# Optimization experiments

Measured on AMD Instinct MI355X. Metric: run time of the kernel, lower is better.

## Reference

```python
import jax, jax.numpy as jnp
import numpy as np

N = 1_000_000
DATA_DIM = 16
N_COND = 8            # conditions 1..8; condition 0 uses the base model (id 0)
N_BUCKETS = 8         # uniform time intervals per condition on [0,1)
N_MODELS = N_COND * N_BUCKETS + 1   # 65, matches num_models+1 in the torch ctor
HIDDEN = 6            # SimpleModel(data_dim, hidden=6, time_embed_dim=6)
IN_DIM = DATA_DIM + 1 # MLP input is cat([data, t], dim=1)


def setup_inputs() -> dict:
    key = jax.random.key(0)
    k_data, k_cond, k_t, k_w1, k_b1, k_w2, k_b2 = jax.random.split(key, 7)
    data = jax.random.normal(k_data, (N, DATA_DIM), dtype=jnp.float32)
    cond = jax.random.randint(k_cond, (N, 1), 0, N_COND + 1).astype(jnp.float32)  # 0..8
    t = jax.random.uniform(k_t, (N, 1), dtype=jnp.float32)                        # [0,1)
    x = jnp.concatenate([data, cond, t], axis=1)  # [N, DATA_DIM+2]
    s1 = 1.0 / np.sqrt(IN_DIM)
    s2 = 1.0 / np.sqrt(HIDDEN)
    W1 = jax.random.uniform(k_w1, (N_MODELS, IN_DIM, HIDDEN), jnp.float32, -s1, s1)
    b1 = jax.random.uniform(k_b1, (N_MODELS, HIDDEN), jnp.float32, -s1, s1)
    W2 = jax.random.uniform(k_w2, (N_MODELS, HIDDEN, DATA_DIM), jnp.float32, -s2, s2)
    b2 = jax.random.uniform(k_b2, (N_MODELS, DATA_DIM), jnp.float32, -s2, s2)
    return {"x": x, "W1": W1, "b1": b1, "W2": W2, "b2": b2}


def _route(cond_f, t):
    # Bucket routing: cond 0 -> model 0 on [0,1); cond c>=1 -> models 1 + (c-1)*8 + floor(t*8).
    # Equivalent to the torch per-(c, [t1,t2)) masked dispatch with uniform breakpoints.
    c = cond_f.astype(jnp.int32)
    bucket = jnp.clip(jnp.floor(t * N_BUCKETS).astype(jnp.int32), 0, N_BUCKETS - 1)
    return jnp.where(c == 0, 0, 1 + (c - 1) * N_BUCKETS + bucket)


def reference(x, W1, b1, W2, b2):
    data = x[:, :-2]
    cond = x[:, -2]
    t = x[:, -1]
    mid = _route(cond, t)                                   # [N] expert id per row
    xin = jnp.concatenate([data, t[:, None]], axis=1)       # [N, IN_DIM]
    # Fused gather-MLP: gather each row's tiny expert weights and apply the 2-layer MLP.
    h = jax.nn.relu(jnp.einsum('ni,nih->nh', xin, W1[mid]) + b1[mid])   # [N, HIDDEN]
    out = jnp.einsum('nh,nhd->nd', h, W2[mid]) + b2[mid]                # [N, DATA_DIM]
    return out
```

## Files before the change

kernel.cpp:

```cpp
#include <hip/hip_runtime.h>


#define NMODELS 65
#define WPM 220
#define NCHUNK 55
#define BLOCK 1024

__global__ __launch_bounds__(BLOCK, 8) void mvf_kernel(
    const float* __restrict__ x,
    const float* __restrict__ W1,
    const float* __restrict__ b1,
    const float* __restrict__ W2,
    const float* __restrict__ b2,
    float* __restrict__ out,
    int npts)
{
    __shared__ float4 wlds[NCHUNK][NMODELS];
    const int tid = threadIdx.x;

    float* wf = (float*)wlds;
    for (int e = tid; e < NMODELS * WPM; e += BLOCK) {
        const int m = e / WPM, k = e % WPM;
        float v;
        if (k < 102)      v = W1[m * 102 + k];
        else if (k < 108) v = b1[m * 6 + (k - 102)];
        else if (k < 204) v = W2[m * 96 + (k - 108)];
        else              v = b2[m * 16 + (k - 204)];
        wf[(k >> 2) * (NMODELS * 4) + m * 4 + (k & 3)] = v;
    }
    __syncthreads();

    const int p = blockIdx.x * BLOCK + tid;
    if (p >= npts) return;

    float xf[18];
    const float2* xr = (const float2*)(x + (long)p * 18);
    #pragma unroll
    for (int i = 0; i < 9; ++i) {
        float2 v = xr[i];
        xf[2 * i]     = v.x;
        xf[2 * i + 1] = v.y;
    }
    const float t = xf[17];
    const int c = (int)xf[16];
    int bucket = (int)floorf(t * 8.0f);
    bucket = bucket < 0 ? 0 : (bucket > 7 ? 7 : bucket);
    const int mid = (c == 0) ? 0 : 1 + (c - 1) * 8 + bucket;

    float h[6];
    {
        float4 c24 = wlds[24][mid];
        float4 c25 = wlds[25][mid];
        float4 c26 = wlds[26][mid];
        h[0] = fmaf(t, c24.x, c25.z);
        h[1] = fmaf(t, c24.y, c25.w);
        h[2] = fmaf(t, c24.z, c26.x);
        h[3] = fmaf(t, c24.w, c26.y);
        h[4] = fmaf(t, c25.x, c26.z);
        h[5] = fmaf(t, c25.y, c26.w);
    }
    #pragma unroll
    for (int r = 0; r < 8; ++r) {
        float4 a = wlds[3 * r + 0][mid];
        float4 b = wlds[3 * r + 1][mid];
        float4 d = wlds[3 * r + 2][mid];
        const float x0 = xf[2 * r], x1 = xf[2 * r + 1];
        h[0] = fmaf(x0, a.x, h[0]);
        h[1] = fmaf(x0, a.y, h[1]);
        h[2] = fmaf(x0, a.z, h[2]);
        h[3] = fmaf(x0, a.w, h[3]);
        h[4] = fmaf(x0, b.x, h[4]);
        h[5] = fmaf(x0, b.y, h[5]);
        h[0] = fmaf(x1, b.z, h[0]);
        h[1] = fmaf(x1, b.w, h[1]);
        h[2] = fmaf(x1, d.x, h[2]);
        h[3] = fmaf(x1, d.y, h[3]);
        h[4] = fmaf(x1, d.z, h[4]);
        h[5] = fmaf(x1, d.w, h[5]);
    }
    #pragma unroll
    for (int j = 0; j < 6; ++j) h[j] = h[j] > 0.0f ? h[j] : 0.0f;

    float o[16];
    #pragma unroll
    for (int q = 0; q < 4; ++q) {
        float4 v = wlds[51 + q][mid];
        o[4 * q + 0] = v.x;
        o[4 * q + 1] = v.y;
        o[4 * q + 2] = v.z;
        o[4 * q + 3] = v.w;
    }
    #pragma unroll
    for (int j = 0; j < 6; ++j) {
        const float hj = h[j];
        #pragma unroll
        for (int q = 0; q < 4; ++q) {
            float4 v = wlds[27 + 4 * j + q][mid];
            o[4 * q + 0] = fmaf(hj, v.x, o[4 * q + 0]);
            o[4 * q + 1] = fmaf(hj, v.y, o[4 * q + 1]);
            o[4 * q + 2] = fmaf(hj, v.z, o[4 * q + 2]);
            o[4 * q + 3] = fmaf(hj, v.w, o[4 * q + 3]);
        }
    }

    float4* orow = (float4*)(out + (long)p * 16);
    #pragma unroll
    for (int q = 0; q < 4; ++q) {
        orow[q] = make_float4(o[4 * q], o[4 * q + 1], o[4 * q + 2], o[4 * q + 3]);
    }
}

extern "C" void kernel_launch(void* const* d_in, const int* in_sizes, int n_in,
                              void* d_out, int out_size, void* d_ws, size_t ws_size,
                              hipStream_t stream) {
    const float* x  = (const float*)d_in[0];
    const float* W1 = (const float*)d_in[1];
    const float* b1 = (const float*)d_in[2];
    const float* W2 = (const float*)d_in[3];
    const float* b2 = (const float*)d_in[4];
    float* out = (float*)d_out;

    const int npts = in_sizes[0] / 18;
    const int grid = (npts + BLOCK - 1) / BLOCK;
    mvf_kernel<<<grid, BLOCK, 0, stream>>>(x, W1, b1, W2, b2, out, npts);
}
```

Baseline: 44.87 us.

## Sort rows by expert within block to make LDS weight reads uniform

Each block first reads only the cond/t columns, builds a per-model histogram with LDS atomics, prefix-sums it serially, and permutes row indices so that adjacent threads share the same expert. The intent is to turn divergent per-thread LDS gathers across 65 models into near-broadcast reads that avoid bank conflicts. In exchange it adds three extra barriers, a serial scan by one thread, scattered global row reads and writes (each thread now handles a non-adjacent row), and a reduced launch-bounds occupancy hint.

```diff
diff --git a/kernel.cpp b/kernel.cpp
--- a/kernel.cpp
+++ b/kernel.cpp
@@ -6,7 +6,7 @@
 #define NCHUNK 55
 #define BLOCK 1024
 
-__global__ __launch_bounds__(BLOCK, 8) void mvf_kernel(
+__global__ __launch_bounds__(BLOCK, 4) void mvf_kernel(
     const float* __restrict__ x,
     const float* __restrict__ W1,
     const float* __restrict__ b1,
@@ -16,7 +16,19 @@
     int npts)
 {
     __shared__ float4 wlds[NCHUNK][NMODELS];
+    __shared__ unsigned bidx[BLOCK];
+    __shared__ int hist[NMODELS];
+    __shared__ int base[NMODELS];
+
     const int tid = threadIdx.x;
+    if (tid < NMODELS) hist[tid] = 0;
+
+    const long pbase = (long)blockIdx.x * BLOCK;
+    const int nvalid = min(BLOCK, npts - (int)pbase);
+    const bool valid = tid < nvalid;
+
+    float2 ct = make_float2(0.0f, 0.0f);
+    if (valid) ct = *(const float2*)(x + (pbase + tid) * 18 + 16);
 
     float* wf = (float*)wlds;
     for (int e = tid; e < NMODELS * WPM; e += BLOCK) {
@@ -30,11 +42,34 @@
     }
     __syncthreads();
 
-    const int p = blockIdx.x * BLOCK + tid;
-    if (p >= npts) return;
+    int mid = 0, myoff = 0;
+    if (valid) {
+        const int c = (int)ct.x;
+        const float t = ct.y;
+        int bucket = (int)floorf(t * 8.0f);
+        bucket = bucket < 0 ? 0 : (bucket > 7 ? 7 : bucket);
+        mid = (c == 0) ? 0 : 1 + (c - 1) * 8 + bucket;
+        myoff = atomicAdd(&hist[mid], 1);
+    }
+    __syncthreads();
 
+    if (tid == 0) {
+        int acc = 0;
+        for (int m = 0; m < NMODELS; ++m) { base[m] = acc; acc += hist[m]; }
+    }
+    __syncthreads();
+
+    if (valid) bidx[base[mid] + myoff] = ((unsigned)mid << 16) | (unsigned)tid;
+    __syncthreads();
+
+    if (!valid) return;
+
+    const unsigned en = bidx[tid];
+    const int src = (int)(en & 0xffffu);
+    const int pm  = (int)(en >> 16);
+
+    const float2* xr = (const float2*)(x + (pbase + src) * 18);
     float xf[18];
-    const float2* xr = (const float2*)(x + (long)p * 18);
     #pragma unroll
     for (int i = 0; i < 9; ++i) {
         float2 v = xr[i];
@@ -42,16 +77,14 @@
         xf[2 * i + 1] = v.y;
     }
     const float t = xf[17];
-    const int c = (int)xf[16];
-    int bucket = (int)floorf(t * 8.0f);
-    bucket = bucket < 0 ? 0 : (bucket > 7 ? 7 : bucket);
-    const int mid = (c == 0) ? 0 : 1 + (c - 1) * 8 + bucket;
+
+    #define CH(cc) wlds[cc][pm]
 
     float h[6];
     {
-        float4 c24 = wlds[24][mid];
-        float4 c25 = wlds[25][mid];
-        float4 c26 = wlds[26][mid];
+        float4 c24 = CH(24);
+        float4 c25 = CH(25);
+        float4 c26 = CH(26);
         h[0] = fmaf(t, c24.x, c25.z);
         h[1] = fmaf(t, c24.y, c25.w);
         h[2] = fmaf(t, c24.z, c26.x);
@@ -61,9 +94,9 @@
     }
     #pragma unroll
     for (int r = 0; r < 8; ++r) {
-        float4 a = wlds[3 * r + 0][mid];
-        float4 b = wlds[3 * r + 1][mid];
-        float4 d = wlds[3 * r + 2][mid];
+        float4 a = CH(3 * r + 0);
+        float4 b = CH(3 * r + 1);
+        float4 d = CH(3 * r + 2);
         const float x0 = xf[2 * r], x1 = xf[2 * r + 1];
         h[0] = fmaf(x0, a.x, h[0]);
         h[1] = fmaf(x0, a.y, h[1]);
@@ -83,31 +116,31 @@
 
     float o[16];
     #pragma unroll
-    for (int q = 0; q < 4; ++q) {
-        float4 v = wlds[51 + q][mid];
-        o[4 * q + 0] = v.x;
-        o[4 * q + 1] = v.y;
-        o[4 * q + 2] = v.z;
-        o[4 * q + 3] = v.w;
+    for (int g = 0; g < 4; ++g) {
+        float4 v = CH(51 + g);
+        o[4 * g + 0] = v.x;
+        o[4 * g + 1] = v.y;
+        o[4 * g + 2] = v.z;
+        o[4 * g + 3] = v.w;
     }
     #pragma unroll
     for (int j = 0; j < 6; ++j) {
         const float hj = h[j];
         #pragma unroll
-        for (int q = 0; q < 4; ++q) {
-            float4 v = wlds[27 + 4 * j + q][mid];
-            o[4 * q + 0] = fmaf(hj, v.x, o[4 * q + 0]);
-            o[4 * q + 1] = fmaf(hj, v.y, o[4 * q + 1]);
-            o[4 * q + 2] = fmaf(hj, v.z, o[4 * q + 2]);
-            o[4 * q + 3] = fmaf(hj, v.w, o[4 * q + 3]);
+        for (int g = 0; g < 4; ++g) {
+            float4 v = CH(27 + 4 * j + g);
+            o[4 * g + 0] = fmaf(hj, v.x, o[4 * g + 0]);
+            o[4 * g + 1] = fmaf(hj, v.y, o[4 * g + 1]);
+            o[4 * g + 2] = fmaf(hj, v.z, o[4 * g + 2]);
+            o[4 * g + 3] = fmaf(hj, v.w, o[4 * g + 3]);
         }
     }
+    #undef CH
 
-    float4* orow = (float4*)(out + (long)p * 16);
+    float4* orow = (float4*)(out + (pbase + src) * 16);
     #pragma unroll
-    for (int q = 0; q < 4; ++q) {
-        orow[q] = make_float4(o[4 * q], o[4 * q + 1], o[4 * q + 2], o[4 * q + 3]);
-    }
+    for (int g = 0; g < 4; ++g)
+        orow[g] = make_float4(o[4 * g], o[4 * g + 1], o[4 * g + 2], o[4 * g + 3]);
 }
 
 extern "C" void kernel_launch(void* const* d_in, const int* in_sizes, int n_in,
```

Result: slower. 62.13 us (+38.5%).
